# Kernel optimization log

Hardware: AMD Instinct MI355X
Metric: run time of the kernel (lower is better)

The kernel has to match this reference:

```python
import jax, jax.numpy as jnp
import numpy as np

D_MODEL, N_HEADS, D_K, BASE, EPS = 1024, 16, 64, 10000, 1e-6
SCALE = 1.0 / np.sqrt(D_K)


def rope(x):
    # x: [b, s, h, d]
    b, s, h, d = x.shape
    d2 = d // 2
    theta = 1.0 / (BASE ** (jnp.arange(0, d, 2, dtype=jnp.float32) / d))  # [d2]
    idx_theta = jnp.arange(s, dtype=jnp.float32)[:, None] * theta[None, :]  # [s, d2]
    idx_theta2 = jnp.concatenate([idx_theta, idx_theta], axis=1)  # [s, d]
    cos = jnp.cos(idx_theta2)[None, :, None, :]
    sin = jnp.sin(idx_theta2)[None, :, None, :]
    neg_half = jnp.concatenate([-x[..., d2:], x[..., :d2]], axis=-1)
    return x * cos + neg_half * sin


def setup_inputs() -> dict:
    key = jax.random.key(0)
    ks = jax.random.split(key, 10)
    B, S = 2, 2048
    std = 1.0 / np.sqrt(D_MODEL)
    return {
        "h": jax.random.normal(ks[0], (B, S, D_MODEL), dtype=jnp.float32),
        "wq": jax.random.normal(ks[1], (D_MODEL, N_HEADS * D_K), dtype=jnp.float32) * std,
        "bq": jnp.zeros((N_HEADS * D_K,), dtype=jnp.float32),
        "wk": jax.random.normal(ks[2], (D_MODEL, N_HEADS * D_K), dtype=jnp.float32) * std,
        "bk": jnp.zeros((N_HEADS * D_K,), dtype=jnp.float32),
        "wv": jax.random.normal(ks[3], (D_MODEL, N_HEADS * D_K), dtype=jnp.float32) * std,
        "bv": jnp.zeros((N_HEADS * D_K,), dtype=jnp.float32),
        "wo": jax.random.normal(ks[4], (N_HEADS * D_K, D_MODEL), dtype=jnp.float32) * std,
        "bo": jnp.zeros((D_MODEL,), dtype=jnp.float32),
        "g": jnp.ones((D_MODEL,), dtype=jnp.float32),
    }


def reference(h, wq, bq, wk, bk, wv, bv, wo, bo, g):
    B, S, _ = h.shape
    h_res = h
    # RMSNorm
    hn = h * jax.lax.rsqrt(jnp.mean(h * h, axis=-1, keepdims=True) + EPS) * g
    mh = (B, S, N_HEADS, D_K)
    q = (hn @ wq + bq).reshape(mh)
    k = (hn @ wk + bk).reshape(mh)
    v = (hn @ wv + bv).reshape(mh)
    q, k = rope(q), rope(k)
    attn = jnp.einsum('bihd,bjhd->bhij', q, k) * SCALE
    mask = jnp.tril(jnp.ones((S, S), dtype=bool))
    attn = jnp.where(mask, attn, -jnp.inf)
    attn = jax.nn.softmax(attn, axis=-1)
    out = jnp.einsum('bhij,bjhd->bihd', attn, v).reshape(B, S, N_HEADS * D_K)
    return out @ wo + bo + h_res
```

## Files before the change

kernel.cpp:

```cpp
#include <hip/hip_runtime.h>
#include <hip/hip_bf16.h>

#define D_MODEL 1024
#define NH 16
#define DK 64
#define SEQ 2048
#define BATCH 2
#define NTOK (BATCH * SEQ)
#define EPS 1e-6f

typedef __attribute__((ext_vector_type(4))) float f32x4;
typedef __attribute__((ext_vector_type(16))) float f32x16;
typedef __attribute__((ext_vector_type(8))) short s16x8;
typedef unsigned int u32;
typedef __hip_bfloat16 bf16;

#define AS1 __attribute__((address_space(1)))
#define AS3 __attribute__((address_space(3)))

static __device__ __forceinline__ s16x8 ld8(const bf16* p) {
    return *reinterpret_cast<const s16x8*>(p);
}
static __device__ __forceinline__ float b2f(short s) {
    return __uint_as_float(((u32)(unsigned short)s) << 16);
}

static __device__ __forceinline__ u32 cvtpk(float lo, float hi) {
    u32 r;
    asm volatile("v_cvt_pk_bf16_f32 %0, %1, %2" : "=v"(r) : "v"(lo), "v"(hi));
    return r;
}
static __device__ __forceinline__ void swap32(u32& a, u32& b) {
    asm volatile("v_permlane32_swap_b32 %0, %1" : "+v"(a), "+v"(b));
}
static __device__ __forceinline__ float exp2f_fast(float x) {
    float r;
    asm("v_exp_f32 %0, %1" : "=v"(r) : "v"(x));
    return r;
}
static __device__ __forceinline__ void gld_lds16(const bf16* g, bf16* l) {
    __builtin_amdgcn_global_load_lds((const AS1 void*)g, (AS3 void*)l, 16, 0, 0);
}

union W4 { s16x8 v; u32 w[4]; };

#define LDSW(arr, row, kc) ld8(&arr[(row)][(((kc) ^ ((row) & 7)) << 3)])

__global__ __launch_bounds__(256) void k_rmsnorm(const float* __restrict__ h,
                                                 const float* __restrict__ g,
                                                 bf16* __restrict__ hn,
                                                 float2* __restrict__ tab) {
    const int row = blockIdx.x;
    const int tid = threadIdx.x;
    const float4 x = reinterpret_cast<const float4*>(h + (size_t)row * D_MODEL)[tid];
    float ss = x.x * x.x + x.y * x.y + x.z * x.z + x.w * x.w;
#pragma unroll
    for (int off = 32; off; off >>= 1) ss += __shfl_xor(ss, off);
    __shared__ float red[4];
    if ((tid & 63) == 0) red[tid >> 6] = ss;
    __syncthreads();
    const float tot = red[0] + red[1] + red[2] + red[3];
    const float rs = rsqrtf(tot * (1.0f / D_MODEL) + EPS);
    const float4 gg = reinterpret_cast<const float4*>(g)[tid];
    bf16* o = hn + (size_t)row * D_MODEL + tid * 4;
    o[0] = __float2bfloat16(x.x * rs * gg.x);
    o[1] = __float2bfloat16(x.y * rs * gg.y);
    o[2] = __float2bfloat16(x.z * rs * gg.z);
    o[3] = __float2bfloat16(x.w * rs * gg.w);
    if (row < 256) {
        const int idx = row * 256 + tid;
        const int s = idx >> 5, i = idx & 31;
        const float theta = __expf(-(float)i * 0.28782313662425572f);
        float sn, cs;
        sincosf((float)s * theta, &sn, &cs);
        tab[idx] = make_float2(cs, sn);
    }
}

__global__ __launch_bounds__(256) void k_packT4(const float* __restrict__ wq,
                                                const float* __restrict__ wk,
                                                const float* __restrict__ wv,
                                                const float* __restrict__ wo,
                                                bf16* __restrict__ dst) {
    __shared__ float t[32][33];
    const int kt = blockIdx.x * 32;
    const int nt = blockIdx.y * 32;
    const float* W = (blockIdx.y < 32) ? wq : (blockIdx.y < 64) ? wk
                   : (blockIdx.y < 96) ? wv : wo;
    const int nl = nt & (D_MODEL - 1);
    const int tx = threadIdx.x, ty = threadIdx.y;
#pragma unroll
    for (int i = 0; i < 4; i++)
        t[ty + 8 * i][tx] = W[(size_t)(kt + ty + 8 * i) * D_MODEL + nl + tx];
    __syncthreads();
#pragma unroll
    for (int i = 0; i < 4; i++)
        dst[(size_t)(nt + ty + 8 * i) * D_MODEL + kt + tx] = __float2bfloat16(t[tx][ty + 8 * i]);
}

__global__ __launch_bounds__(256) void k_gemm64_qkv(const bf16* __restrict__ A,
                                                    const bf16* __restrict__ Bt,
                                                    const float* __restrict__ bq,
                                                    const float* __restrict__ bk,
                                                    const float* __restrict__ bv,
                                                    const float2* __restrict__ tab,
                                                    bf16* __restrict__ qb,
                                                    bf16* __restrict__ kpk,
                                                    bf16* __restrict__ vpk) {
    __shared__ __align__(16) char smem[16384];
    bf16(*As)[64] = (bf16(*)[64])smem;
    bf16(*Bs)[64] = (bf16(*)[64])(smem + 8192);
    const int tid = threadIdx.x;
    const int w = tid >> 6, lane = tid & 63, l16 = lane & 15, lq = lane >> 4;
    const int wr = w >> 1, wc = w & 1;
    const int col0 = blockIdx.x * 64;
    const int row0 = blockIdx.y * 64;
    const int grow = lane >> 3;
    const int scol = (((lane & 7) ^ grow) << 3);
    f32x4 acc[2][2];
#pragma unroll
    for (int i = 0; i < 2; i++)
#pragma unroll
        for (int j = 0; j < 2; j++) acc[i][j] = f32x4{0, 0, 0, 0};

    for (int kt = 0; kt < D_MODEL; kt += 64) {
        gld_lds16(A + (size_t)(row0 + w * 16 + grow) * D_MODEL + kt + scol,      &As[w * 16][0]);
        gld_lds16(A + (size_t)(row0 + w * 16 + 8 + grow) * D_MODEL + kt + scol,  &As[w * 16 + 8][0]);
        gld_lds16(Bt + (size_t)(col0 + w * 16 + grow) * D_MODEL + kt + scol,     &Bs[w * 16][0]);
        gld_lds16(Bt + (size_t)(col0 + w * 16 + 8 + grow) * D_MODEL + kt + scol, &Bs[w * 16 + 8][0]);
        __syncthreads();
        s16x8 af[2][2], bfr[2][2];
#pragma unroll
        for (int mi = 0; mi < 2; mi++)
#pragma unroll
            for (int ks = 0; ks < 2; ks++)
                af[mi][ks] = LDSW(As, wr * 32 + mi * 16 + l16, ks * 4 + lq);
#pragma unroll
        for (int ni = 0; ni < 2; ni++)
#pragma unroll
            for (int ks = 0; ks < 2; ks++)
                bfr[ni][ks] = LDSW(Bs, wc * 32 + ni * 16 + l16, ks * 4 + lq);
        __builtin_amdgcn_s_setprio(1);
#pragma unroll
        for (int ks = 0; ks < 2; ks++)
#pragma unroll
            for (int mi = 0; mi < 2; mi++)
#pragma unroll
                for (int ni = 0; ni < 2; ni++)
                    acc[mi][ni] = __builtin_amdgcn_mfma_f32_16x16x32_bf16(af[mi][ks], bfr[ni][ks], acc[mi][ni], 0, 0, 0);
        __builtin_amdgcn_s_setprio(0);
        __syncthreads();
    }

    const int sect = col0 >> 10;
    const int b_ = row0 >> 11;
    const int head = (col0 & 1023) >> 6;
    if (sect == 2) {
        const int e0 = (lq & 1) * 4;
        const int tileL = (row0 & (SEQ - 1)) >> 6;
        bf16* dstH = vpk + ((size_t)(b_ * NH + head) << 17);
#pragma unroll
        for (int ni = 0; ni < 2; ni++) {
            const int dloc = wc * 32 + ni * 16 + l16;
            const float bs = bv[(col0 & 1023) + dloc];
#pragma unroll
            for (int mi = 0; mi < 2; mi++) {
                const int m = wr * 2 + mi;
                size_t off = ((((size_t)(tileL * 2 + (dloc >> 5)) * 4 + m) * 64
                               + ((lq >> 1) & 1) * 32 + (dloc & 31)) << 3) + e0;
                uint2 pv;
                pv.x = cvtpk(acc[mi][ni][0] + bs, acc[mi][ni][1] + bs);
                pv.y = cvtpk(acc[mi][ni][2] + bs, acc[mi][ni][3] + bs);
                *reinterpret_cast<uint2*>(dstH + off) = pv;
            }
        }
        return;
    }
    bf16(*Cs)[72] = (bf16(*)[72])smem;
    const float* bias = (sect == 0) ? bq : bk;
#pragma unroll
    for (int ni = 0; ni < 2; ni++) {
        const int cl = wc * 32 + ni * 16 + l16;
        const float bs = bias[(col0 & 1023) + cl];
#pragma unroll
        for (int mi = 0; mi < 2; mi++) {
            const int rl = wr * 32 + mi * 16 + lq * 4;
#pragma unroll
            for (int r = 0; r < 4; r++)
                Cs[rl + r][cl] = __float2bfloat16(acc[mi][ni][r] + bs);
        }
    }
    __syncthreads();
    const int row = tid >> 2, q = tid & 3;
    const int s_ = (row0 + row) & (SEQ - 1);
    const float2* tb = tab + s_ * 32 + q * 8;
    const float qs = (sect == 0) ? 0.18033688011112042f : 1.0f;
    const s16x8 vlo = ld8(&Cs[row][q * 8]);
    const s16x8 vhi = ld8(&Cs[row][q * 8 + 32]);
    u32 plo[4], phi[4];
#pragma unroll
    for (int e2 = 0; e2 < 4; e2++) {
        float a[2], b[2];
#pragma unroll
        for (int k = 0; k < 2; k++) {
            const int e = e2 * 2 + k;
            const float2 cs = tb[e];
            const float x1 = b2f(vlo[e]), x2 = b2f(vhi[e]);
            a[k] = (x1 * cs.x - x2 * cs.y) * qs;
            b[k] = (x2 * cs.x + x1 * cs.y) * qs;
        }
        plo[e2] = cvtpk(a[0], a[1]);
        phi[e2] = cvtpk(b[0], b[1]);
    }
    if (sect == 0) {
        bf16* qdst = qb + (((size_t)(b_ * NH + head) * SEQ + s_) << 6);
        *reinterpret_cast<uint4*>(qdst + q * 8)      = make_uint4(plo[0], plo[1], plo[2], plo[3]);
        *reinterpret_cast<uint4*>(qdst + 32 + q * 8) = make_uint4(phi[0], phi[1], phi[2], phi[3]);
    } else {
        bf16* kdst = kpk + ((size_t)(b_ * NH + head) << 17);
        const int jb = s_ >> 5, j31 = s_ & 31;
        const size_t offL = (((size_t)(jb * 4 + (q >> 1)) * 64 + (q & 1) * 32 + j31) << 3);
        const size_t offH = (((size_t)(jb * 4 + ((q + 4) >> 1)) * 64 + ((q + 4) & 1) * 32 + j31) << 3);
        *reinterpret_cast<uint4*>(kdst + offL) = make_uint4(plo[0], plo[1], plo[2], plo[3]);
        *reinterpret_cast<uint4*>(kdst + offH) = make_uint4(phi[0], phi[1], phi[2], phi[3]);
    }
}

__global__ __launch_bounds__(256) void k_attn5(const bf16* __restrict__ qg,
                                               const bf16* __restrict__ kp,
                                               const bf16* __restrict__ vp,
                                               bf16* __restrict__ ao) {
    __shared__ float part[2][64][36];
    const int tid = threadIdx.x;
    const int wid = tid >> 6;
    const int lane = tid & 63;
    const int l31 = lane & 31;
    const int hi = lane >> 5;
    const int pi = wid >> 1;
    const int h = wid & 1;
    const int bid = blockIdx.x;
    const int blk = (bid >> 3) & 31;
    const int bh  = (bid & 7) + ((bid >> 8) << 3);
    const int pos = pi ? (63 - blk) : blk;
    const int qw = pos << 5;
    const int qrow = qw + l31;

    const bf16* qptr = qg + (((size_t)bh * SEQ + qrow) << 6) + 8 * hi;
    s16x8 qf[4];
#pragma unroll
    for (int t = 0; t < 4; t++) qf[t] = ld8(qptr + 16 * t);

    f32x16 o0, o1;
#pragma unroll
    for (int r = 0; r < 16; r++) { o0[r] = 0.0f; o1[r] = 0.0f; }
    float m_run = -1e30f, l_run = 0.0f;

    const int nfull = qw >> 6;
    const int ntot  = (qw + 95) >> 6;
    const int kt0 = h ? (ntot >> 1) : 0;
    const int kt1 = h ? ntot : (ntot >> 1);
    const bf16* kbase = kp + ((size_t)bh << 17);
    const bf16* vbase = vp + ((size_t)bh << 17);

    s16x8 kA[8], kB[8], vC[8];

    auto att_step = [&](s16x8(&KC)[8], s16x8(&KN)[8], const int kt) {
        const int kb = kt << 6;
#pragma unroll
        for (int t = 0; t < 8; t++)
            vC[t] = ld8(vbase + (((size_t)(kt * 8 + t) * 64 + lane) << 3));
        f32x16 s0, s1;
#pragma unroll
        for (int r = 0; r < 16; r++) { s0[r] = 0.0f; s1[r] = 0.0f; }
        __builtin_amdgcn_s_setprio(1);
#pragma unroll
        for (int t = 0; t < 4; t++) {
            s0 = __builtin_amdgcn_mfma_f32_32x32x16_bf16(KC[t],     qf[t], s0, 0, 0, 0);
            s1 = __builtin_amdgcn_mfma_f32_32x32x16_bf16(KC[4 + t], qf[t], s1, 0, 0, 0);
        }
        __builtin_amdgcn_s_setprio(0);
        const int ktn = (kt + 1 < kt1) ? kt + 1 : kt;
#pragma unroll
        for (int t = 0; t < 8; t++)
            KN[t] = ld8(kbase + (((size_t)(ktn * 8 + t) * 64 + lane) << 3));
        float p[32];
#pragma unroll
        for (int r = 0; r < 16; r++) { p[r] = s0[r]; p[16 + r] = s1[r]; }
        if (kt >= nfull) {
#pragma unroll
            for (int r = 0; r < 32; r++) {
                const int j = kb + 8 * (r >> 2) + (r & 3) + 4 * hi;
                if (j > qrow) p[r] = -3.0e38f;
            }
        }
        float m16[16];
#pragma unroll
        for (int r = 0; r < 16; r++) m16[r] = fmaxf(p[r], p[r + 16]);
#pragma unroll
        for (int r = 0; r < 8; r++) m16[r] = fmaxf(m16[r], m16[r + 8]);
#pragma unroll
        for (int r = 0; r < 4; r++) m16[r] = fmaxf(m16[r], m16[r + 4]);
        float mx = fmaxf(fmaxf(m16[0], m16[1]), fmaxf(m16[2], m16[3]));
        mx = fmaxf(mx, __shfl_xor(mx, 32));
        if (!__all(mx <= m_run + 8.0f)) {
            const float mn = fmaxf(m_run, mx);
            const float alpha = exp2f_fast(m_run - mn);
            m_run = mn;
            l_run *= alpha;
#pragma unroll
            for (int r = 0; r < 16; r++) { o0[r] *= alpha; o1[r] *= alpha; }
        }
        float s4[4] = {0, 0, 0, 0};
#pragma unroll
        for (int r = 0; r < 32; r++) { p[r] = exp2f_fast(p[r] - m_run); s4[r & 3] += p[r]; }
        float rs = (s4[0] + s4[1]) + (s4[2] + s4[3]);
        rs += __shfl_xor(rs, 32);
        l_run += rs;
        u32 pk_[16];
#pragma unroll
        for (int a = 0; a < 8; a++) {
            pk_[2 * a]     = cvtpk(p[4 * a],     p[4 * a + 1]);
            pk_[2 * a + 1] = cvtpk(p[4 * a + 2], p[4 * a + 3]);
        }
        __builtin_amdgcn_s_setprio(1);
#pragma unroll
        for (int m = 0; m < 4; m++) {
            u32 b0 = pk_[4 * m],     b2 = pk_[4 * m + 2];
            u32 b1 = pk_[4 * m + 1], b3 = pk_[4 * m + 3];
            swap32(b0, b2);
            swap32(b1, b3);
            W4 B; B.w[0] = b0; B.w[1] = b1; B.w[2] = b2; B.w[3] = b3;
            o0 = __builtin_amdgcn_mfma_f32_32x32x16_bf16(vC[m],     B.v, o0, 0, 0, 0);
            o1 = __builtin_amdgcn_mfma_f32_32x32x16_bf16(vC[4 + m], B.v, o1, 0, 0, 0);
        }
        __builtin_amdgcn_s_setprio(0);
    };

    int kt = kt0;
    if (kt < kt1) {
#pragma unroll
        for (int t = 0; t < 8; t++) kA[t] = ld8(kbase + (((size_t)(kt * 8 + t) * 64 + lane) << 3));
        for (;;) {
            att_step(kA, kB, kt); if (++kt == kt1) break;
            att_step(kB, kA, kt); if (++kt == kt1) break;
        }
    }

    if (h == 0) {
        float* dst = &part[pi][lane][0];
#pragma unroll
        for (int r4 = 0; r4 < 4; r4++) {
            *reinterpret_cast<float4*>(dst + r4 * 4) =
                make_float4(o0[4 * r4], o0[4 * r4 + 1], o0[4 * r4 + 2], o0[4 * r4 + 3]);
            *reinterpret_cast<float4*>(dst + 16 + r4 * 4) =
                make_float4(o1[4 * r4], o1[4 * r4 + 1], o1[4 * r4 + 2], o1[4 * r4 + 3]);
        }
        dst[32] = m_run;
        dst[33] = l_run;
    }
    __syncthreads();
    if (h == 0) return;

    const float* src = &part[pi][lane][0];
    const float mA = src[32], lA = src[33];
    const float mN = fmaxf(mA, m_run);
    const float aA = exp2f_fast(mA - mN);
    const float aB = exp2f_fast(m_run - mN);
    const float inv = 1.0f / (lA * aA + l_run * aB);

    const int b_ = bh >> 4, h_ = bh & (NH - 1);
    bf16* orow = ao + (((size_t)(b_ * SEQ + qrow)) << 10) + (h_ << 6);
#pragma unroll
    for (int g = 0; g < 4; g++) {
        {
            uint2 val;
            val.x = cvtpk((src[4 * g] * aA + o0[4 * g] * aB) * inv,
                          (src[4 * g + 1] * aA + o0[4 * g + 1] * aB) * inv);
            val.y = cvtpk((src[4 * g + 2] * aA + o0[4 * g + 2] * aB) * inv,
                          (src[4 * g + 3] * aA + o0[4 * g + 3] * aB) * inv);
            *reinterpret_cast<uint2*>(orow + 8 * g + 4 * hi) = val;
        }
        {
            uint2 val;
            val.x = cvtpk((src[16 + 4 * g] * aA + o1[4 * g] * aB) * inv,
                          (src[16 + 4 * g + 1] * aA + o1[4 * g + 1] * aB) * inv);
            val.y = cvtpk((src[16 + 4 * g + 2] * aA + o1[4 * g + 2] * aB) * inv,
                          (src[16 + 4 * g + 3] * aA + o1[4 * g + 3] * aB) * inv);
            *reinterpret_cast<uint2*>(orow + 32 + 8 * g + 4 * hi) = val;
        }
    }
}

__global__ __launch_bounds__(256) void k_gemm64_out(const bf16* __restrict__ A,
                                                    const bf16* __restrict__ Bt,
                                                    const float* __restrict__ bo,
                                                    const float* __restrict__ hres,
                                                    float* __restrict__ out) {
    __shared__ __align__(16) char smem[16384];
    bf16(*As)[64] = (bf16(*)[64])smem;
    bf16(*Bs)[64] = (bf16(*)[64])(smem + 8192);
    const int tid = threadIdx.x;
    const int w = tid >> 6, lane = tid & 63, l16 = lane & 15, lq = lane >> 4;
    const int wr = w >> 1, wc = w & 1;
    const int col0 = blockIdx.x * 64;
    const int row0 = blockIdx.y * 64;
    const int grow = lane >> 3;
    const int scol = (((lane & 7) ^ grow) << 3);
    f32x4 acc[2][2];
#pragma unroll
    for (int i = 0; i < 2; i++)
#pragma unroll
        for (int j = 0; j < 2; j++) acc[i][j] = f32x4{0, 0, 0, 0};

    for (int kt = 0; kt < D_MODEL; kt += 64) {
        gld_lds16(A + (size_t)(row0 + w * 16 + grow) * D_MODEL + kt + scol,      &As[w * 16][0]);
        gld_lds16(A + (size_t)(row0 + w * 16 + 8 + grow) * D_MODEL + kt + scol,  &As[w * 16 + 8][0]);
        gld_lds16(Bt + (size_t)(col0 + w * 16 + grow) * D_MODEL + kt + scol,     &Bs[w * 16][0]);
        gld_lds16(Bt + (size_t)(col0 + w * 16 + 8 + grow) * D_MODEL + kt + scol, &Bs[w * 16 + 8][0]);
        __syncthreads();
        s16x8 af[2][2], bfr[2][2];
#pragma unroll
        for (int mi = 0; mi < 2; mi++)
#pragma unroll
            for (int ks = 0; ks < 2; ks++)
                af[mi][ks] = LDSW(As, wr * 32 + mi * 16 + l16, ks * 4 + lq);
#pragma unroll
        for (int ni = 0; ni < 2; ni++)
#pragma unroll
            for (int ks = 0; ks < 2; ks++)
                bfr[ni][ks] = LDSW(Bs, wc * 32 + ni * 16 + l16, ks * 4 + lq);
        __builtin_amdgcn_s_setprio(1);
#pragma unroll
        for (int ks = 0; ks < 2; ks++)
#pragma unroll
            for (int mi = 0; mi < 2; mi++)
#pragma unroll
                for (int ni = 0; ni < 2; ni++)
                    acc[mi][ni] = __builtin_amdgcn_mfma_f32_16x16x32_bf16(af[mi][ks], bfr[ni][ks], acc[mi][ni], 0, 0, 0);
        __builtin_amdgcn_s_setprio(0);
        __syncthreads();
    }
#pragma unroll
    for (int ni = 0; ni < 2; ni++) {
        const int col = col0 + wc * 32 + ni * 16 + l16;
        const float bs = bo[col];
#pragma unroll
        for (int mi = 0; mi < 2; mi++) {
#pragma unroll
            for (int r = 0; r < 4; r++) {
                const int row = row0 + wr * 32 + mi * 16 + lq * 4 + r;
                out[(size_t)row * D_MODEL + col] =
                    acc[mi][ni][r] + bs + hres[(size_t)row * D_MODEL + col];
            }
        }
    }
}

extern "C" void kernel_launch(void* const* d_in, const int* in_sizes, int n_in,
                              void* d_out, int out_size, void* d_ws, size_t ws_size,
                              hipStream_t stream) {
    (void)in_sizes; (void)n_in; (void)out_size; (void)ws_size;
    const float* h  = (const float*)d_in[0];
    const float* wq = (const float*)d_in[1];
    const float* bq = (const float*)d_in[2];
    const float* wk = (const float*)d_in[3];
    const float* bk = (const float*)d_in[4];
    const float* wv = (const float*)d_in[5];
    const float* bv = (const float*)d_in[6];
    const float* wo = (const float*)d_in[7];
    const float* bo = (const float*)d_in[8];
    const float* g  = (const float*)d_in[9];
    float* out = (float*)d_out;

    char* ws = (char*)d_ws;
    size_t off = 0;
    auto carve = [&](size_t bytes) {
        void* p = ws + off;
        off += (bytes + 255) & ~(size_t)255;
        return p;
    };
    bf16* hn    = (bf16*)carve((size_t)NTOK * D_MODEL * 2);
    bf16* wallT = (bf16*)carve((size_t)4 * D_MODEL * D_MODEL * 2);
    bf16* wqkvT = wallT;
    bf16* woT   = wallT + (size_t)3 * D_MODEL * D_MODEL;
    bf16* qb    = (bf16*)carve((size_t)BATCH * NH * SEQ * DK * 2);
    bf16* kpk   = (bf16*)carve((size_t)BATCH * NH * SEQ * DK * 2);
    bf16* vpk   = (bf16*)carve((size_t)BATCH * NH * SEQ * DK * 2);
    bf16* ao    = (bf16*)carve((size_t)NTOK * D_MODEL * 2);
    float2* tab = (float2*)carve((size_t)SEQ * 32 * sizeof(float2));

    k_rmsnorm<<<NTOK, 256, 0, stream>>>(h, g, hn, tab);
    k_packT4<<<dim3(32, 128), dim3(32, 8), 0, stream>>>(wq, wk, wv, wo, wallT);
    k_gemm64_qkv<<<dim3(48, 64), 256, 0, stream>>>(hn, wqkvT, bq, bk, bv, tab, qb, kpk, vpk);
    k_attn5<<<1024, 256, 0, stream>>>(qb, kpk, vpk, ao);
    k_gemm64_out<<<dim3(16, 64), 256, 0, stream>>>(ao, woT, bo, h, out);
}
```

Measured before the change: 122.3 us.

## Merge rmsnorm and weight pack kernels; interleave attention KV tiles between wave halves

Fuses the RMSNorm/RoPE-table kernel and the weight transpose-pack kernel into one launch, choosing the branch by block index, which removes one kernel launch. In attention, each block now takes adjacent query tiles (2*pb+pi) in place of mirrored ones, and the two split-K waves walk KV tiles in even/odd order instead of splitting the range into contiguous halves. This balances the causal work between the two waves more evenly, but it drops the mirrored pairing that balanced load across blocks. The LDS partial buffer row stride also changes from 36 to 35 floats.

```diff
diff --git a/kernel.cpp b/kernel.cpp
--- a/kernel.cpp
+++ b/kernel.cpp
@@ -46,56 +46,59 @@
 
 #define LDSW(arr, row, kc) ld8(&arr[(row)][(((kc) ^ ((row) & 7)) << 3)])
 
-__global__ __launch_bounds__(256) void k_rmsnorm(const float* __restrict__ h,
-                                                 const float* __restrict__ g,
-                                                 bf16* __restrict__ hn,
-                                                 float2* __restrict__ tab) {
-    const int row = blockIdx.x;
+__global__ __launch_bounds__(256) void k_prep(const float* __restrict__ h,
+                                              const float* __restrict__ g,
+                                              const float* __restrict__ wq,
+                                              const float* __restrict__ wk,
+                                              const float* __restrict__ wv,
+                                              const float* __restrict__ wo,
+                                              bf16* __restrict__ hn,
+                                              bf16* __restrict__ wallT,
+                                              float2* __restrict__ tab) {
+    const int bid = blockIdx.x;
     const int tid = threadIdx.x;
-    const float4 x = reinterpret_cast<const float4*>(h + (size_t)row * D_MODEL)[tid];
-    float ss = x.x * x.x + x.y * x.y + x.z * x.z + x.w * x.w;
-#pragma unroll
-    for (int off = 32; off; off >>= 1) ss += __shfl_xor(ss, off);
-    __shared__ float red[4];
-    if ((tid & 63) == 0) red[tid >> 6] = ss;
-    __syncthreads();
-    const float tot = red[0] + red[1] + red[2] + red[3];
-    const float rs = rsqrtf(tot * (1.0f / D_MODEL) + EPS);
-    const float4 gg = reinterpret_cast<const float4*>(g)[tid];
-    bf16* o = hn + (size_t)row * D_MODEL + tid * 4;
-    o[0] = __float2bfloat16(x.x * rs * gg.x);
-    o[1] = __float2bfloat16(x.y * rs * gg.y);
-    o[2] = __float2bfloat16(x.z * rs * gg.z);
-    o[3] = __float2bfloat16(x.w * rs * gg.w);
-    if (row < 256) {
-        const int idx = row * 256 + tid;
-        const int s = idx >> 5, i = idx & 31;
-        const float theta = __expf(-(float)i * 0.28782313662425572f);
-        float sn, cs;
-        sincosf((float)s * theta, &sn, &cs);
-        tab[idx] = make_float2(cs, sn);
-    }
-}
-
-__global__ __launch_bounds__(256) void k_packT4(const float* __restrict__ wq,
-                                                const float* __restrict__ wk,
-                                                const float* __restrict__ wv,
-                                                const float* __restrict__ wo,
-                                                bf16* __restrict__ dst) {
-    __shared__ float t[32][33];
-    const int kt = blockIdx.x * 32;
-    const int nt = blockIdx.y * 32;
-    const float* W = (blockIdx.y < 32) ? wq : (blockIdx.y < 64) ? wk
-                   : (blockIdx.y < 96) ? wv : wo;
-    const int nl = nt & (D_MODEL - 1);
-    const int tx = threadIdx.x, ty = threadIdx.y;
-#pragma unroll
-    for (int i = 0; i < 4; i++)
-        t[ty + 8 * i][tx] = W[(size_t)(kt + ty + 8 * i) * D_MODEL + nl + tx];
-    __syncthreads();
-#pragma unroll
-    for (int i = 0; i < 4; i++)
-        dst[(size_t)(nt + ty + 8 * i) * D_MODEL + kt + tx] = __float2bfloat16(t[tx][ty + 8 * i]);
+    if (bid < 4096) {
+        const int row = bid;
+        const float4 x = reinterpret_cast<const float4*>(h + (size_t)row * D_MODEL)[tid];
+        float ss = x.x * x.x + x.y * x.y + x.z * x.z + x.w * x.w;
+#pragma unroll
+        for (int off = 32; off; off >>= 1) ss += __shfl_xor(ss, off);
+        __shared__ float red[4];
+        if ((tid & 63) == 0) red[tid >> 6] = ss;
+        __syncthreads();
+        const float tot = red[0] + red[1] + red[2] + red[3];
+        const float rs = rsqrtf(tot * (1.0f / D_MODEL) + EPS);
+        const float4 gg = reinterpret_cast<const float4*>(g)[tid];
+        bf16* o = hn + (size_t)row * D_MODEL + tid * 4;
+        o[0] = __float2bfloat16(x.x * rs * gg.x);
+        o[1] = __float2bfloat16(x.y * rs * gg.y);
+        o[2] = __float2bfloat16(x.z * rs * gg.z);
+        o[3] = __float2bfloat16(x.w * rs * gg.w);
+        if (row < 256) {
+            const int idx = row * 256 + tid;
+            const int s = idx >> 5, i = idx & 31;
+            const float theta = __expf(-(float)i * 0.28782313662425572f);
+            float sn, cs;
+            sincosf((float)s * theta, &sn, &cs);
+            tab[idx] = make_float2(cs, sn);
+        }
+    } else {
+        __shared__ float t[32][33];
+        const int bid2 = bid - 4096;
+        const int kt = (bid2 & 31) * 32;
+        const int by = bid2 >> 5;
+        const int nt = by * 32;
+        const float* W = (by < 32) ? wq : (by < 64) ? wk : (by < 96) ? wv : wo;
+        const int nl = nt & (D_MODEL - 1);
+        const int tx = tid & 31, ty = tid >> 5;
+#pragma unroll
+        for (int i = 0; i < 4; i++)
+            t[ty + 8 * i][tx] = W[(size_t)(kt + ty + 8 * i) * D_MODEL + nl + tx];
+        __syncthreads();
+#pragma unroll
+        for (int i = 0; i < 4; i++)
+            wallT[(size_t)(nt + ty + 8 * i) * D_MODEL + kt + tx] = __float2bfloat16(t[tx][ty + 8 * i]);
+    }
 }
 
 __global__ __launch_bounds__(256) void k_gemm64_qkv(const bf16* __restrict__ A,
@@ -226,11 +229,11 @@
     }
 }
 
-__global__ __launch_bounds__(256) void k_attn5(const bf16* __restrict__ qg,
+__global__ __launch_bounds__(256) void k_attn7(const bf16* __restrict__ qg,
                                                const bf16* __restrict__ kp,
                                                const bf16* __restrict__ vp,
                                                bf16* __restrict__ ao) {
-    __shared__ float part[2][64][36];
+    __shared__ float part[2][64][35];
     const int tid = threadIdx.x;
     const int wid = tid >> 6;
     const int lane = tid & 63;
@@ -239,9 +242,9 @@
     const int pi = wid >> 1;
     const int h = wid & 1;
     const int bid = blockIdx.x;
-    const int blk = (bid >> 3) & 31;
+    const int pb  = (bid >> 3) & 31;
     const int bh  = (bid & 7) + ((bid >> 8) << 3);
-    const int pos = pi ? (63 - blk) : blk;
+    const int pos = 2 * pb + pi;
     const int qw = pos << 5;
     const int qrow = qw + l31;
 
@@ -257,8 +260,6 @@
 
     const int nfull = qw >> 6;
     const int ntot  = (qw + 95) >> 6;
-    const int kt0 = h ? (ntot >> 1) : 0;
-    const int kt1 = h ? ntot : (ntot >> 1);
     const bf16* kbase = kp + ((size_t)bh << 17);
     const bf16* vbase = vp + ((size_t)bh << 17);
 
@@ -279,7 +280,7 @@
             s1 = __builtin_amdgcn_mfma_f32_32x32x16_bf16(KC[4 + t], qf[t], s1, 0, 0, 0);
         }
         __builtin_amdgcn_s_setprio(0);
-        const int ktn = (kt + 1 < kt1) ? kt + 1 : kt;
+        const int ktn = (kt + 2 < ntot) ? kt + 2 : kt;
 #pragma unroll
         for (int t = 0; t < 8; t++)
             KN[t] = ld8(kbase + (((size_t)(ktn * 8 + t) * 64 + lane) << 3));
@@ -336,13 +337,13 @@
         __builtin_amdgcn_s_setprio(0);
     };
 
-    int kt = kt0;
-    if (kt < kt1) {
+    int kt = h;
+    if (kt < ntot) {
 #pragma unroll
         for (int t = 0; t < 8; t++) kA[t] = ld8(kbase + (((size_t)(kt * 8 + t) * 64 + lane) << 3));
         for (;;) {
-            att_step(kA, kB, kt); if (++kt == kt1) break;
-            att_step(kB, kA, kt); if (++kt == kt1) break;
+            att_step(kA, kB, kt); kt += 2; if (kt >= ntot) break;
+            att_step(kB, kA, kt); kt += 2; if (kt >= ntot) break;
         }
     }
 
@@ -489,9 +490,8 @@
     bf16* ao    = (bf16*)carve((size_t)NTOK * D_MODEL * 2);
     float2* tab = (float2*)carve((size_t)SEQ * 32 * sizeof(float2));
 
-    k_rmsnorm<<<NTOK, 256, 0, stream>>>(h, g, hn, tab);
-    k_packT4<<<dim3(32, 128), dim3(32, 8), 0, stream>>>(wq, wk, wv, wo, wallT);
+    k_prep<<<8192, 256, 0, stream>>>(h, g, wq, wk, wv, wo, hn, wallT, tab);
     k_gemm64_qkv<<<dim3(48, 64), 256, 0, stream>>>(hn, wqkvT, bq, bk, bv, tab, qb, kpk, vpk);
-    k_attn5<<<1024, 256, 0, stream>>>(qb, kpk, vpk, ao);
+    k_attn7<<<1024, 256, 0, stream>>>(qb, kpk, vpk, ao);
     k_gemm64_out<<<dim3(16, 64), 256, 0, stream>>>(ao, woT, bo, h, out);
 }
```

Measured after the change: 120.1 us. About the same (-1.8%).
